# Optimization experiments

Measured on AMD Instinct MI355X. Metric: run time of the kernel, lower is better.

Reference implementation:

```python
import jax, jax.numpy as jnp
import numpy as np

TOPK = 20

def setup_inputs() -> dict:
    key = jax.random.key(0)
    k1, k2, k3 = jax.random.split(key, 3)
    B, n, D = 4, 4096, 256
    src1 = jax.random.normal(k1, (B, n, D), dtype=jnp.float32)
    src2 = jax.random.normal(k2, (B, n, D), dtype=jnp.float32)
    memoryMartix = jax.random.normal(k3, (n, n), dtype=jnp.float32)
    return {"src1": src1, "src2": src2, "memoryMartix": memoryMartix}

def reference(src1, src2, memoryMartix):
    # softmax over dim=1 of the [n, n] memory matrix
    probs = jax.nn.softmax(memoryMartix, axis=1)            # [n, n]
    # top-k along dim=1: values and indices per row
    vtopk, ind = jax.lax.top_k(probs, TOPK)                 # [n, k], [n, k]
    # gather src2 rows per output position: [B, n, k, D]
    gathered = jnp.take(src2, ind, axis=1)
    # weighted sum over the k selected neighbors
    src = jnp.einsum('bnkd,nk->bnd', gathered, vtopk)       # [B, n, D]
    return src + src1
```

## Files before the change

kernel.cpp:

```cpp
#include <hip/hip_runtime.h>
#include <math.h>

#define TOPK  20
#define NROW  4096
#define DDIM  256
#define NB    4

#define HCHUNK 8
#define ABLOCK 256
#define BBLOCK 256

typedef float vf4 __attribute__((ext_vector_type(4)));

__device__ __forceinline__ bool lex_gt(float av, int ai, float bv, int bi) {
    return (av > bv) || (av == bv && ai < bi);
}

__device__ __forceinline__ void bitonic64_desc(float& v, int& i, int lane) {
#pragma unroll
    for (int k = 2; k <= 64; k <<= 1) {
#pragma unroll
        for (int j = k >> 1; j > 0; j >>= 1) {
            float pv = __shfl_xor(v, j, 64);
            int   pi = __shfl_xor(i, j, 64);
            bool takeBig = ((lane & k) == 0) == ((lane & j) == 0);
            bool pBig = lex_gt(pv, pi, v, i);
            if (takeBig == pBig) { v = pv; i = pi; }
        }
    }
}

__global__ __launch_bounds__(ABLOCK) void topk_select(
    const float* __restrict__ mem,
    float* __restrict__ ws_w,
    int*   __restrict__ ws_i)
{
    __shared__ float mv[2][2][TOPK];
    __shared__ int   mi[2][2][TOPK];
    __shared__ float mstat[2][2][2];
    __shared__ float cand_v[4][64];
    __shared__ int   cand_i[4][64];

    const int wave   = threadIdx.x >> 6;
    const int lane   = threadIdx.x & 63;
    const int rowloc = wave >> 1;
    const int half   = wave & 1;
    const int n      = blockIdx.x * 2 + rowloc;
    const int off    = half * (NROW / 2);

    const float4* hrow = (const float4*)(mem + (size_t)n * NROW + off);
    float4 v4[HCHUNK];
#pragma unroll
    for (int j = 0; j < HCHUNK; ++j) v4[j] = hrow[lane + 64 * j];

    float bv = -INFINITY; int bi = 0x7fffffff;
#pragma unroll
    for (int j = 0; j < HCHUNK; ++j) {
        const int base = off + 4 * lane + 256 * j;
        if (v4[j].x > bv) { bv = v4[j].x; bi = base + 0; }
        if (v4[j].y > bv) { bv = v4[j].y; bi = base + 1; }
        if (v4[j].z > bv) { bv = v4[j].z; bi = base + 2; }
        if (v4[j].w > bv) { bv = v4[j].w; bi = base + 3; }
    }

    float sv = bv; int si = bi;
    bitonic64_desc(sv, si, lane);
    const float hmax = __shfl(sv, 0, 64);
    const float tv   = __shfl(sv, 19, 64);
    const int   ti   = __shfl(si, 19, 64);

    float lsum = 0.f;
#pragma unroll
    for (int j = 0; j < HCHUNK; ++j) {
        lsum += __expf(v4[j].x - hmax) + __expf(v4[j].y - hmax)
              + __expf(v4[j].z - hmax) + __expf(v4[j].w - hmax);
    }
#pragma unroll
    for (int o = 32; o > 0; o >>= 1) lsum += __shfl_xor(lsum, o, 64);

    int cnt = 0;
#pragma unroll
    for (int j = 0; j < HCHUNK; ++j) {
        const int base = off + 4 * lane + 256 * j;
        cnt += (v4[j].x > tv) || (v4[j].x == tv && (base + 0) <= ti);
        cnt += (v4[j].y > tv) || (v4[j].y == tv && (base + 1) <= ti);
        cnt += (v4[j].z > tv) || (v4[j].z == tv && (base + 2) <= ti);
        cnt += (v4[j].w > tv) || (v4[j].w == tv && (base + 3) <= ti);
    }
    int incl = cnt;
#pragma unroll
    for (int o = 1; o < 64; o <<= 1) {
        int t = __shfl_up(incl, o, 64);
        if (lane >= o) incl += t;
    }
    const int total = __builtin_amdgcn_readfirstlane(__shfl(incl, 63, 64));

    if (total <= 64) {
        int o2 = incl - cnt;
#pragma unroll
        for (int j = 0; j < HCHUNK; ++j) {
            const int base = off + 4 * lane + 256 * j;
            const float4 q = v4[j];
            if ((q.x > tv) || (q.x == tv && (base + 0) <= ti)) { cand_v[wave][o2] = q.x; cand_i[wave][o2] = base + 0; ++o2; }
            if ((q.y > tv) || (q.y == tv && (base + 1) <= ti)) { cand_v[wave][o2] = q.y; cand_i[wave][o2] = base + 1; ++o2; }
            if ((q.z > tv) || (q.z == tv && (base + 2) <= ti)) { cand_v[wave][o2] = q.z; cand_i[wave][o2] = base + 2; ++o2; }
            if ((q.w > tv) || (q.w == tv && (base + 3) <= ti)) { cand_v[wave][o2] = q.w; cand_i[wave][o2] = base + 3; ++o2; }
        }
        asm volatile("s_waitcnt lgkmcnt(0)" ::: "memory");
        float cv = -INFINITY; int ci = 0x7fffffff;
        if (lane < total) { cv = cand_v[wave][lane]; ci = cand_i[wave][lane]; }
        bitonic64_desc(cv, ci, lane);
        if (lane < TOPK) { mv[rowloc][half][lane] = cv; mi[rowloc][half][lane] = ci; }
    } else {
        unsigned dead = 0;
        float cv = bv; int ci = bi;
        for (int r = 0; r < TOPK; ++r) {
            float wv = cv; int wi = ci;
#pragma unroll
            for (int o = 32; o > 0; o >>= 1) {
                float ov = __shfl_xor(wv, o, 64);
                int   oi = __shfl_xor(wi, o, 64);
                if (lex_gt(ov, oi, wv, wi)) { wv = ov; wi = oi; }
            }
            if (lane == 0) { mv[rowloc][half][r] = wv; mi[rowloc][half][r] = wi; }
            if (ci == wi) {
                const int local = wi - off;
                dead |= (1u << (4 * (local >> 8) + (local & 3)));
                cv = -INFINITY; ci = 0x7fffffff;
#pragma unroll
                for (int j = 0; j < HCHUNK; ++j) {
                    const int base = off + 4 * lane + 256 * j;
                    if (!((dead >> (4 * j + 0)) & 1) && v4[j].x > cv) { cv = v4[j].x; ci = base + 0; }
                    if (!((dead >> (4 * j + 1)) & 1) && v4[j].y > cv) { cv = v4[j].y; ci = base + 1; }
                    if (!((dead >> (4 * j + 2)) & 1) && v4[j].z > cv) { cv = v4[j].z; ci = base + 2; }
                    if (!((dead >> (4 * j + 3)) & 1) && v4[j].w > cv) { cv = v4[j].w; ci = base + 3; }
                }
            }
        }
    }
    if (lane == 0) { mstat[rowloc][half][0] = hmax; mstat[rowloc][half][1] = lsum; }
    __syncthreads();

    if (half == 0) {
        float cv = -INFINITY; int ci = 0x7fffffff;
        if (lane < 2 * TOPK) {
            const int h = lane >= TOPK;
            const int k = h ? lane - TOPK : lane;
            cv = mv[rowloc][h][k];
            ci = mi[rowloc][h][k];
        }
        bitonic64_desc(cv, ci, lane);

        const float m0 = mstat[rowloc][0][0], s0 = mstat[rowloc][0][1];
        const float m1 = mstat[rowloc][1][0], s1 = mstat[rowloc][1][1];
        const float M  = fmaxf(m0, m1);
        const float S  = s0 * __expf(m0 - M) + s1 * __expf(m1 - M);
        const float invS = 1.0f / S;

        if (lane < TOPK) {
            ws_w[(size_t)n * TOPK + lane] = __expf(cv - M) * invS;
            ws_i[(size_t)n * TOPK + lane] = ci;
        }
    }
}

__global__ __launch_bounds__(BBLOCK, 4) void gather_epilogue(
    const float* __restrict__ src1,
    const float* __restrict__ src2,
    const float* __restrict__ ws_w,
    const int*   __restrict__ ws_i,
    float* __restrict__ out)
{
    const int bid    = blockIdx.x;
    const int b      = (bid & 7) >> 1;
    const int ngroup = ((bid >> 3) << 1) | (bid & 1);
    const int wave   = threadIdx.x >> 6;
    const int lane   = threadIdx.x & 63;
    const int n      = ngroup * 4 + wave;

    const float* gw = ws_w + (size_t)n * TOPK;
    const int*   gi = ws_i + (size_t)n * TOPK;
    float wk[TOPK]; int ik[TOPK];
#pragma unroll
    for (int k = 0; k < TOPK; ++k) { wk[k] = gw[k]; ik[k] = gi[k]; }

    const vf4* s1  = (const vf4*)src1;
    const vf4* s2b = (const vf4*)src2 + (size_t)b * NROW * (DDIM / 4);
    vf4*       o4  = (vf4*)out;

    const size_t rowbase = ((size_t)b * NROW + n) * (DDIM / 4) + lane;
    vf4 acc = __builtin_nontemporal_load(s1 + rowbase);
#pragma unroll
    for (int k = 0; k < TOPK; ++k) {
        const vf4 g = s2b[(size_t)ik[k] * (DDIM / 4) + lane];
        acc += wk[k] * g;
    }
    __builtin_nontemporal_store(acc, o4 + rowbase);
}

extern "C" void kernel_launch(void* const* d_in, const int* in_sizes, int n_in,
                              void* d_out, int out_size, void* d_ws, size_t ws_size,
                              hipStream_t stream) {
    const float* src1 = (const float*)d_in[0];
    const float* src2 = (const float*)d_in[1];
    const float* mem  = (const float*)d_in[2];
    float* out = (float*)d_out;

    float* ws_w = (float*)d_ws;
    int*   ws_i = (int*)d_ws + (size_t)NROW * TOPK;

    topk_select<<<NROW / 2, ABLOCK, 0, stream>>>(mem, ws_w, ws_i);
    gather_epilogue<<<NROW, BBLOCK, 0, stream>>>(src1, src2, ws_w, ws_i, out);
}
```

Before: 152.6 us.

## Move top-k half merge and softmax normalisation into gather kernel

The top-k kernel now writes each half-row's 20 candidates plus max/sum stats to workspace and no longer synchronises within the block to merge halves. The gather kernel merges the 40 candidates with a wave bitonic sort, computes the softmax normalisation, and stages weights in shared memory. This removes the __syncthreads and idle half-waves from the selection kernel. In exchange, the merge is repeated for each of the 4 batch blocks that touch a row, and the launch-bounds occupancy hint on the gather kernel is dropped.

```diff
diff --git a/kernel.cpp b/kernel.cpp
--- a/kernel.cpp
+++ b/kernel.cpp
@@ -30,23 +30,21 @@
     }
 }
 
-__global__ __launch_bounds__(ABLOCK) void topk_select(
+__global__ __launch_bounds__(ABLOCK) void topk_half(
     const float* __restrict__ mem,
-    float* __restrict__ ws_w,
-    int*   __restrict__ ws_i)
+    float* __restrict__ ws_v,
+    int*   __restrict__ ws_idx,
+    float* __restrict__ ws_s)
 {
-    __shared__ float mv[2][2][TOPK];
-    __shared__ int   mi[2][2][TOPK];
-    __shared__ float mstat[2][2][2];
     __shared__ float cand_v[4][64];
     __shared__ int   cand_i[4][64];
 
-    const int wave   = threadIdx.x >> 6;
-    const int lane   = threadIdx.x & 63;
-    const int rowloc = wave >> 1;
-    const int half   = wave & 1;
-    const int n      = blockIdx.x * 2 + rowloc;
-    const int off    = half * (NROW / 2);
+    const int wave  = threadIdx.x >> 6;
+    const int lane  = threadIdx.x & 63;
+    const int gwave = blockIdx.x * 4 + wave;
+    const int n     = gwave >> 1;
+    const int half  = gwave & 1;
+    const int off   = half * (NROW / 2);
 
     const float4* hrow = (const float4*)(mem + (size_t)n * NROW + off);
     float4 v4[HCHUNK];
@@ -94,6 +92,9 @@
         if (lane >= o) incl += t;
     }
     const int total = __builtin_amdgcn_readfirstlane(__shfl(incl, 63, 64));
+
+    float* gv = ws_v   + (size_t)n * (2 * TOPK) + half * TOPK;
+    int*   gi = ws_idx + (size_t)n * (2 * TOPK) + half * TOPK;
 
     if (total <= 64) {
         int o2 = incl - cnt;
@@ -110,7 +111,7 @@
         float cv = -INFINITY; int ci = 0x7fffffff;
         if (lane < total) { cv = cand_v[wave][lane]; ci = cand_i[wave][lane]; }
         bitonic64_desc(cv, ci, lane);
-        if (lane < TOPK) { mv[rowloc][half][lane] = cv; mi[rowloc][half][lane] = ci; }
+        if (lane < TOPK) { gv[lane] = cv; gi[lane] = ci; }
     } else {
         unsigned dead = 0;
         float cv = bv; int ci = bi;
@@ -122,7 +123,7 @@
                 int   oi = __shfl_xor(wi, o, 64);
                 if (lex_gt(ov, oi, wv, wi)) { wv = ov; wi = oi; }
             }
-            if (lane == 0) { mv[rowloc][half][r] = wv; mi[rowloc][half][r] = wi; }
+            if (lane == 0) { gv[r] = wv; gi[r] = wi; }
             if (ci == wi) {
                 const int local = wi - off;
                 dead |= (1u << (4 * (local >> 8) + (local & 3)));
@@ -138,39 +139,23 @@
             }
         }
     }
-    if (lane == 0) { mstat[rowloc][half][0] = hmax; mstat[rowloc][half][1] = lsum; }
-    __syncthreads();
-
-    if (half == 0) {
-        float cv = -INFINITY; int ci = 0x7fffffff;
-        if (lane < 2 * TOPK) {
-            const int h = lane >= TOPK;
-            const int k = h ? lane - TOPK : lane;
-            cv = mv[rowloc][h][k];
-            ci = mi[rowloc][h][k];
-        }
-        bitonic64_desc(cv, ci, lane);
-
-        const float m0 = mstat[rowloc][0][0], s0 = mstat[rowloc][0][1];
-        const float m1 = mstat[rowloc][1][0], s1 = mstat[rowloc][1][1];
-        const float M  = fmaxf(m0, m1);
-        const float S  = s0 * __expf(m0 - M) + s1 * __expf(m1 - M);
-        const float invS = 1.0f / S;
-
-        if (lane < TOPK) {
-            ws_w[(size_t)n * TOPK + lane] = __expf(cv - M) * invS;
-            ws_i[(size_t)n * TOPK + lane] = ci;
-        }
-    }
-}
-
-__global__ __launch_bounds__(BBLOCK, 4) void gather_epilogue(
+    if (lane == 0) {
+        ws_s[(size_t)n * 4 + half * 2 + 0] = hmax;
+        ws_s[(size_t)n * 4 + half * 2 + 1] = lsum;
+    }
+}
+
+__global__ __launch_bounds__(BBLOCK) void gather_epilogue(
     const float* __restrict__ src1,
     const float* __restrict__ src2,
-    const float* __restrict__ ws_w,
-    const int*   __restrict__ ws_i,
+    const float* __restrict__ ws_v,
+    const int*   __restrict__ ws_idx,
+    const float* __restrict__ ws_s,
     float* __restrict__ out)
 {
+    __shared__ float bw[4][TOPK];
+    __shared__ int   bidx[4][TOPK];
+
     const int bid    = blockIdx.x;
     const int b      = (bid & 7) >> 1;
     const int ngroup = ((bid >> 3) << 1) | (bid & 1);
@@ -178,18 +163,35 @@
     const int lane   = threadIdx.x & 63;
     const int n      = ngroup * 4 + wave;
 
-    const float* gw = ws_w + (size_t)n * TOPK;
-    const int*   gi = ws_i + (size_t)n * TOPK;
+    float cv = -INFINITY; int ci = 0x7fffffff;
+    if (lane < 2 * TOPK) {
+        cv = ws_v[(size_t)n * (2 * TOPK) + lane];
+        ci = ws_idx[(size_t)n * (2 * TOPK) + lane];
+    }
+    bitonic64_desc(cv, ci, lane);
+
+    const float m0 = ws_s[(size_t)n * 4 + 0], s0 = ws_s[(size_t)n * 4 + 1];
+    const float m1 = ws_s[(size_t)n * 4 + 2], s1 = ws_s[(size_t)n * 4 + 3];
+    const float M  = fmaxf(m0, m1);
+    const float S  = s0 * __expf(m0 - M) + s1 * __expf(m1 - M);
+    const float invS = 1.0f / S;
+
+    if (lane < TOPK) {
+        bw[wave][lane]   = __expf(cv - M) * invS;
+        bidx[wave][lane] = ci;
+    }
+    asm volatile("s_waitcnt lgkmcnt(0)" ::: "memory");
+
     float wk[TOPK]; int ik[TOPK];
 #pragma unroll
-    for (int k = 0; k < TOPK; ++k) { wk[k] = gw[k]; ik[k] = gi[k]; }
-
-    const vf4* s1  = (const vf4*)src1;
+    for (int k = 0; k < TOPK; ++k) { wk[k] = bw[wave][k]; ik[k] = bidx[wave][k]; }
+
+    const vf4* s1v = (const vf4*)src1;
     const vf4* s2b = (const vf4*)src2 + (size_t)b * NROW * (DDIM / 4);
     vf4*       o4  = (vf4*)out;
 
     const size_t rowbase = ((size_t)b * NROW + n) * (DDIM / 4) + lane;
-    vf4 acc = __builtin_nontemporal_load(s1 + rowbase);
+    vf4 acc = __builtin_nontemporal_load(s1v + rowbase);
 #pragma unroll
     for (int k = 0; k < TOPK; ++k) {
         const vf4 g = s2b[(size_t)ik[k] * (DDIM / 4) + lane];
@@ -206,9 +208,10 @@
     const float* mem  = (const float*)d_in[2];
     float* out = (float*)d_out;
 
-    float* ws_w = (float*)d_ws;
-    int*   ws_i = (int*)d_ws + (size_t)NROW * TOPK;
-
-    topk_select<<<NROW / 2, ABLOCK, 0, stream>>>(mem, ws_w, ws_i);
-    gather_epilogue<<<NROW, BBLOCK, 0, stream>>>(src1, src2, ws_w, ws_i, out);
-}
+    float* ws_v   = (float*)d_ws;
+    int*   ws_idx = (int*)((float*)d_ws + (size_t)NROW * 2 * TOPK);
+    float* ws_s   = (float*)((int*)ws_idx + (size_t)NROW * 2 * TOPK);
+
+    topk_half<<<NROW * 2 / 4, ABLOCK, 0, stream>>>(mem, ws_v, ws_idx, ws_s);
+    gather_epilogue<<<NROW, BBLOCK, 0, stream>>>(src1, src2, ws_v, ws_idx, ws_s, out);
+}
```

Result: no change. 153.6 us (+0.7%).
